# Optimization experiments

Hardware: AMD Instinct MI355X
Metric: run time of the kernel (lower is better)

The kernel has to match this reference:

```python
import jax, jax.numpy as jnp
import numpy as np

B = 8388608

def setup_inputs() -> dict:
    key = jax.random.key(0)
    k1, k2 = jax.random.split(key)
    pred = jax.random.normal(k1, (B, 2), dtype=jnp.float32)
    target = jax.random.normal(k2, (B, 2), dtype=jnp.float32)
    return {"pred": pred, "target": target}

def reference(pred, target):
    # per-row 2D Euclidean distance on the first two columns
    d = pred[:, :2] - target[:, :2]          # [B, 2]
    dist = jnp.sqrt(jnp.sum(d * d, axis=1))  # [B]
    # original concatenates onto an initial zeros(1), so mean is over B+1 elems
    n = pred.shape[0]
    loss = jnp.sum(dist) / jnp.asarray(n + 1, dtype=dist.dtype)
    return loss
```

## Files before the change

### kernel.cpp

```cpp
#include <hip/hip_runtime.h>


#define NBLOCKS 4096
#define NTHREADS 256
#define VPT 4

__global__ __launch_bounds__(NTHREADS) void dist_partial(
    const float4* __restrict__ pred,
    const float4* __restrict__ targ,
    float* __restrict__ partials,
    int n4) {
    const int base = blockIdx.x * (NTHREADS * VPT) + threadIdx.x;
    float s = 0.0f;

    if (base + 3 * NTHREADS < n4) {
        float4 p0 = pred[base];
        float4 p1 = pred[base + NTHREADS];
        float4 p2 = pred[base + 2 * NTHREADS];
        float4 p3 = pred[base + 3 * NTHREADS];
        float4 t0 = targ[base];
        float4 t1 = targ[base + NTHREADS];
        float4 t2 = targ[base + 2 * NTHREADS];
        float4 t3 = targ[base + 3 * NTHREADS];
        float dx, dy;
        dx = p0.x - t0.x; dy = p0.y - t0.y; s += sqrtf(dx * dx + dy * dy);
        dx = p0.z - t0.z; dy = p0.w - t0.w; s += sqrtf(dx * dx + dy * dy);
        dx = p1.x - t1.x; dy = p1.y - t1.y; s += sqrtf(dx * dx + dy * dy);
        dx = p1.z - t1.z; dy = p1.w - t1.w; s += sqrtf(dx * dx + dy * dy);
        dx = p2.x - t2.x; dy = p2.y - t2.y; s += sqrtf(dx * dx + dy * dy);
        dx = p2.z - t2.z; dy = p2.w - t2.w; s += sqrtf(dx * dx + dy * dy);
        dx = p3.x - t3.x; dy = p3.y - t3.y; s += sqrtf(dx * dx + dy * dy);
        dx = p3.z - t3.z; dy = p3.w - t3.w; s += sqrtf(dx * dx + dy * dy);
    } else {
        #pragma unroll
        for (int k = 0; k < VPT; ++k) {
            int j = base + k * NTHREADS;
            if (j < n4) {
                float4 p = pred[j];
                float4 t = targ[j];
                float dx0 = p.x - t.x, dy0 = p.y - t.y;
                float dx1 = p.z - t.z, dy1 = p.w - t.w;
                s += sqrtf(dx0 * dx0 + dy0 * dy0) + sqrtf(dx1 * dx1 + dy1 * dy1);
            }
        }
    }

    #pragma unroll
    for (int off = 32; off > 0; off >>= 1)
        s += __shfl_down(s, off, 64);
    __shared__ float smem[NTHREADS / 64];
    int lane = threadIdx.x & 63;
    int wave = threadIdx.x >> 6;
    if (lane == 0) smem[wave] = s;
    __syncthreads();
    if (threadIdx.x == 0) {
        float bsum = 0.0f;
        #pragma unroll
        for (int w = 0; w < NTHREADS / 64; ++w) bsum += smem[w];
        partials[blockIdx.x] = bsum;
    }
}

__global__ __launch_bounds__(NTHREADS) void dist_final(
    const float4* __restrict__ partials4,
    int n4,
    float* __restrict__ out,
    float inv_np1) {
    float acc = 0.0f;
    for (int i = threadIdx.x; i < n4; i += NTHREADS) {
        float4 v = partials4[i];
        acc += (v.x + v.y) + (v.z + v.w);
    }
    #pragma unroll
    for (int off = 32; off > 0; off >>= 1)
        acc += __shfl_down(acc, off, 64);
    __shared__ float smem[NTHREADS / 64];
    int lane = threadIdx.x & 63;
    int wave = threadIdx.x >> 6;
    if (lane == 0) smem[wave] = acc;
    __syncthreads();
    if (threadIdx.x == 0) {
        float sv = 0.0f;
        #pragma unroll
        for (int w = 0; w < NTHREADS / 64; ++w) sv += smem[w];
        out[0] = sv * inv_np1;
    }
}

extern "C" void kernel_launch(void* const* d_in, const int* in_sizes, int n_in,
                              void* d_out, int out_size, void* d_ws, size_t ws_size,
                              hipStream_t stream) {
    const float4* pred = (const float4*)d_in[0];
    const float4* targ = (const float4*)d_in[1];
    float* out = (float*)d_out;
    float* partials = (float*)d_ws;

    long long total_floats = (long long)in_sizes[0];
    long long n_rows = total_floats / 2;
    int n4 = (int)(total_floats / 4);

    float inv_np1 = 1.0f / (float)(n_rows + 1);

    dist_partial<<<NBLOCKS, NTHREADS, 0, stream>>>(pred, targ, partials, n4);
    dist_final<<<1, NTHREADS, 0, stream>>>((const float4*)partials, NBLOCKS / 4,
                                           out, inv_np1);
}
```

Baseline: 26.95 us.

## Halve partial-sum blocks with two-batch loop and single-wave final reduce

Each block of the partial kernel now processes two consecutive 1024-float4 spans in a non-unrolled loop, halving the grid to 2048 blocks and the number of partials. The final reduction runs as a single 64-thread wave using only shuffles, dropping the shared-memory step and barrier. This aims to cut per-block launch and reduction overhead and shorten the tail kernel. The cost is fewer outstanding loads per thread at a time, which could lower memory-level parallelism on a bandwidth-bound kernel.

Result: slower. 29.06 us (+7.8%).

```diff
diff --git a/kernel.cpp b/kernel.cpp
--- a/kernel.cpp
+++ b/kernel.cpp
@@ -1,46 +1,55 @@
 #include <hip/hip_runtime.h>
 
 
-#define NBLOCKS 4096
+#define NBLOCKS 2048
 #define NTHREADS 256
 #define VPT 4
+#define NBATCH 2
 
 __global__ __launch_bounds__(NTHREADS) void dist_partial(
     const float4* __restrict__ pred,
     const float4* __restrict__ targ,
     float* __restrict__ partials,
     int n4) {
-    const int base = blockIdx.x * (NTHREADS * VPT) + threadIdx.x;
+    const int span = NTHREADS * VPT;
+    const int blockBase = blockIdx.x * (span * NBATCH);
     float s = 0.0f;
 
-    if (base + 3 * NTHREADS < n4) {
-        float4 p0 = pred[base];
-        float4 p1 = pred[base + NTHREADS];
-        float4 p2 = pred[base + 2 * NTHREADS];
-        float4 p3 = pred[base + 3 * NTHREADS];
-        float4 t0 = targ[base];
-        float4 t1 = targ[base + NTHREADS];
-        float4 t2 = targ[base + 2 * NTHREADS];
-        float4 t3 = targ[base + 3 * NTHREADS];
-        float dx, dy;
-        dx = p0.x - t0.x; dy = p0.y - t0.y; s += sqrtf(dx * dx + dy * dy);
-        dx = p0.z - t0.z; dy = p0.w - t0.w; s += sqrtf(dx * dx + dy * dy);
-        dx = p1.x - t1.x; dy = p1.y - t1.y; s += sqrtf(dx * dx + dy * dy);
-        dx = p1.z - t1.z; dy = p1.w - t1.w; s += sqrtf(dx * dx + dy * dy);
-        dx = p2.x - t2.x; dy = p2.y - t2.y; s += sqrtf(dx * dx + dy * dy);
-        dx = p2.z - t2.z; dy = p2.w - t2.w; s += sqrtf(dx * dx + dy * dy);
-        dx = p3.x - t3.x; dy = p3.y - t3.y; s += sqrtf(dx * dx + dy * dy);
-        dx = p3.z - t3.z; dy = p3.w - t3.w; s += sqrtf(dx * dx + dy * dy);
+    if (blockBase + span * NBATCH <= n4) {
+        #pragma unroll 1
+        for (int b = 0; b < NBATCH; ++b) {
+            const int base = blockBase + b * span + (int)threadIdx.x;
+            float4 p0 = pred[base];
+            float4 p1 = pred[base + NTHREADS];
+            float4 p2 = pred[base + 2 * NTHREADS];
+            float4 p3 = pred[base + 3 * NTHREADS];
+            float4 t0 = targ[base];
+            float4 t1 = targ[base + NTHREADS];
+            float4 t2 = targ[base + 2 * NTHREADS];
+            float4 t3 = targ[base + 3 * NTHREADS];
+            float dx, dy;
+            dx = p0.x - t0.x; dy = p0.y - t0.y; s += sqrtf(dx * dx + dy * dy);
+            dx = p0.z - t0.z; dy = p0.w - t0.w; s += sqrtf(dx * dx + dy * dy);
+            dx = p1.x - t1.x; dy = p1.y - t1.y; s += sqrtf(dx * dx + dy * dy);
+            dx = p1.z - t1.z; dy = p1.w - t1.w; s += sqrtf(dx * dx + dy * dy);
+            dx = p2.x - t2.x; dy = p2.y - t2.y; s += sqrtf(dx * dx + dy * dy);
+            dx = p2.z - t2.z; dy = p2.w - t2.w; s += sqrtf(dx * dx + dy * dy);
+            dx = p3.x - t3.x; dy = p3.y - t3.y; s += sqrtf(dx * dx + dy * dy);
+            dx = p3.z - t3.z; dy = p3.w - t3.w; s += sqrtf(dx * dx + dy * dy);
+        }
     } else {
-        #pragma unroll
-        for (int k = 0; k < VPT; ++k) {
-            int j = base + k * NTHREADS;
-            if (j < n4) {
-                float4 p = pred[j];
-                float4 t = targ[j];
-                float dx0 = p.x - t.x, dy0 = p.y - t.y;
-                float dx1 = p.z - t.z, dy1 = p.w - t.w;
-                s += sqrtf(dx0 * dx0 + dy0 * dy0) + sqrtf(dx1 * dx1 + dy1 * dy1);
+        for (int b = 0; b < NBATCH; ++b) {
+            #pragma unroll
+            for (int k = 0; k < VPT; ++k) {
+                int j = blockBase + b * span + k * NTHREADS + (int)threadIdx.x;
+                if (j < n4) {
+                    float4 p = pred[j];
+                    float4 t = targ[j];
+                    float dx0 = p.x - t.x, dy0 = p.y - t.y;
+                    float dx1 = p.z - t.z, dy1 = p.w - t.w;
+                    s += sqrtf(dx0 * dx0 + dy0 * dy0) +
+                         sqrtf(dx1 * dx1 + dy1 * dy1);
+                }
             }
         }
     }
@@ -61,30 +70,20 @@
     }
 }
 
-__global__ __launch_bounds__(NTHREADS) void dist_final(
+__global__ __launch_bounds__(64) void dist_final(
     const float4* __restrict__ partials4,
     int n4,
     float* __restrict__ out,
     float inv_np1) {
     float acc = 0.0f;
-    for (int i = threadIdx.x; i < n4; i += NTHREADS) {
+    for (int i = threadIdx.x; i < n4; i += 64) {
         float4 v = partials4[i];
         acc += (v.x + v.y) + (v.z + v.w);
     }
     #pragma unroll
     for (int off = 32; off > 0; off >>= 1)
         acc += __shfl_down(acc, off, 64);
-    __shared__ float smem[NTHREADS / 64];
-    int lane = threadIdx.x & 63;
-    int wave = threadIdx.x >> 6;
-    if (lane == 0) smem[wave] = acc;
-    __syncthreads();
-    if (threadIdx.x == 0) {
-        float sv = 0.0f;
-        #pragma unroll
-        for (int w = 0; w < NTHREADS / 64; ++w) sv += smem[w];
-        out[0] = sv * inv_np1;
-    }
+    if (threadIdx.x == 0) out[0] = acc * inv_np1;
 }
 
 extern "C" void kernel_launch(void* const* d_in, const int* in_sizes, int n_in,
@@ -102,6 +101,6 @@
     float inv_np1 = 1.0f / (float)(n_rows + 1);
 
     dist_partial<<<NBLOCKS, NTHREADS, 0, stream>>>(pred, targ, partials, n4);
-    dist_final<<<1, NTHREADS, 0, stream>>>((const float4*)partials, NBLOCKS / 4,
-                                           out, inv_np1);
+    dist_final<<<1, 64, 0, stream>>>((const float4*)partials, NBLOCKS / 4,
+                                     out, inv_np1);
 }
```
